# Optimization experiments

Measured on AMD Instinct MI355X. Metric: run time of the kernel, lower is better.

The kernel has to match this reference:

```python
import jax, jax.numpy as jnp
import numpy as np

BATCH, T, IN, OUT, N = 8, 2048, 512, 512, 512
DS = 1024  # temporal_downsampling


def setup_inputs() -> dict:
    key = jax.random.key(0)
    ks = jax.random.split(key, 8)
    x = jax.random.normal(ks[0], (BATCH, T, IN), dtype=jnp.float32)
    # LRU ring initialization of eigenvalues lambda = exp(-exp(nu_log) + i*exp(theta_log))
    r_min, r_max = 0.4, 0.99
    u1 = jax.random.uniform(ks[1], (N,), dtype=jnp.float32)
    u2 = jax.random.uniform(ks[2], (N,), dtype=jnp.float32)
    nu_log = jnp.log(-0.5 * jnp.log(u1 * (r_max**2 - r_min**2) + r_min**2))
    theta_log = jnp.log(u2 * (2.0 * np.pi) + 1e-6)
    lam_abs = jnp.exp(-jnp.exp(nu_log))
    gamma_log = jnp.log(jnp.sqrt(1.0 - lam_abs**2))  # input normalization
    B_re = jax.random.normal(ks[3], (N, IN), dtype=jnp.float32) / np.sqrt(2 * IN)
    B_im = jax.random.normal(ks[4], (N, IN), dtype=jnp.float32) / np.sqrt(2 * IN)
    C_re = jax.random.normal(ks[5], (OUT, N), dtype=jnp.float32) / np.sqrt(N)
    C_im = jax.random.normal(ks[6], (OUT, N), dtype=jnp.float32) / np.sqrt(N)
    D = jax.random.normal(ks[7], (OUT, IN), dtype=jnp.float32) / np.sqrt(IN)
    return {"x": x, "nu_log": nu_log, "theta_log": theta_log, "gamma_log": gamma_log,
            "B_re": B_re, "B_im": B_im, "C_re": C_re, "C_im": C_im, "D": D}


def reference(x, nu_log, theta_log, gamma_log, B_re, B_im, C_re, C_im, D):
    # diagonal complex recurrence: h_t = lam * h_{t-1} + gamma * B x_t
    lam = jnp.exp(-jnp.exp(nu_log) + 1j * jnp.exp(theta_log))  # [N] complex64
    gamma = jnp.exp(gamma_log)  # [N]
    # input projection (real GEMMs), then scale: Bu [b, t, n] complex
    Bu = (jnp.einsum('bti,ni->btn', x, B_re)
          + 1j * jnp.einsum('bti,ni->btn', x, B_im)) * gamma
    a = jnp.broadcast_to(lam, Bu.shape)

    def combine(e1, e2):
        a1, b1 = e1
        a2, b2 = e2
        return a1 * a2, a2 * b1 + b2

    _, h = jax.lax.associative_scan(combine, (a, Bu), axis=1)  # h: [b, t, n]
    # y_t = Re(C h_t) + D x_t
    y = (jnp.einsum('btn,on->bto', h.real, C_re)
         - jnp.einsum('btn,on->bto', h.imag, C_im)
         + jnp.einsum('bti,oi->bto', x, D))
    # causal temporal downsampling: keep last DS steps
    return y[:, -DS:]
```

## Files before the change

kernel.cpp:

```cpp
#include <hip/hip_runtime.h>
#include <hip/hip_bf16.h>

typedef __attribute__((ext_vector_type(8))) short bf16x8;
typedef __attribute__((ext_vector_type(16))) float f32x16;

static __device__ __forceinline__ short f2bf(float f) {
    __hip_bfloat16 h = __float2bfloat16(f);
    return *reinterpret_cast<short*>(&h);
}
static __device__ __forceinline__ float bflo(unsigned v) {
    unsigned u = v << 16;
    return *reinterpret_cast<float*>(&u);
}
static __device__ __forceinline__ float bfhi(unsigned v) {
    unsigned u = v & 0xffff0000u;
    return *reinterpret_cast<float*>(&u);
}
static __device__ __forceinline__ unsigned pack2bf(float lo, float hi) {
    return (unsigned)(unsigned short)f2bf(lo) | ((unsigned)(unsigned short)f2bf(hi) << 16);
}

static __device__ __forceinline__ void gload16(const void* g, void* l) {
    __builtin_amdgcn_global_load_lds(
        (const __attribute__((address_space(1))) void*)g,
        (__attribute__((address_space(3))) void*)l, 16, 0, 0);
}

#define BATCH 8
#define TSEQ  2048
#define DS    1024
#define NIN   512
#define NOUT  512
#define NSTATE 512
#define WARM  768
#define TW    (TSEQ - WARM)
#define M1 (BATCH * TW)
#define N1 (2 * NSTATE)
#define K1 NIN
#define M2 (BATCH * DS)
#define N2 NOUT
#define KH 1024
#define K2 (3 * NSTATE)

#define PREP_A 512
#define PREP_B (N1 * K1)
#define PREP_C (N2 * K2)
#define PREP_D (M1 * K1 / 4)
#define PREP_TOT (PREP_A + PREP_B + PREP_C + PREP_D)
__global__ void k_prep(const float* __restrict__ nu_log,
                       const float* __restrict__ theta_log,
                       const float* __restrict__ gamma_log,
                       const float* __restrict__ B_re,
                       const float* __restrict__ B_im,
                       const float* __restrict__ C_re,
                       const float* __restrict__ C_im,
                       const float* __restrict__ D,
                       const float* __restrict__ x,
                       float* __restrict__ consts,
                       short* __restrict__ Bcat,
                       short* __restrict__ Wcat,
                       short* __restrict__ xb) {
    int idx = blockIdx.x * 256 + threadIdx.x;
    if (idx >= PREP_A + PREP_B + PREP_C) {
        int e  = (idx - PREP_A - PREP_B - PREP_C) * 4;
        int m  = e >> 9;
        int i  = e & 511;
        int b  = m / TW;
        int tt = m - b * TW;
        const float4 v = *reinterpret_cast<const float4*>(
            &x[((size_t)(b * TSEQ + WARM + tt) << 9) + i]);
        union { short s[4]; uint2 u; } pk;
        pk.s[0] = f2bf(v.x); pk.s[1] = f2bf(v.y);
        pk.s[2] = f2bf(v.z); pk.s[3] = f2bf(v.w);
        *reinterpret_cast<uint2*>(&xb[e]) = pk.u;
    } else if (idx < PREP_A) {
        int n = idx;
        float mag = expf(-expf(nu_log[n]));
        float th  = expf(theta_log[n]);
        float lre = mag * cosf(th);
        float lim = mag * sinf(th);
        consts[n]          = lre;
        consts[NSTATE + n] = lim;
        float pr = lre, pi = lim;
#pragma unroll
        for (int s = 0; s < 5; ++s) {
            float nr = pr * pr - pi * pi;
            float ni = 2.0f * pr * pi;
            pr = nr; pi = ni;
        }
        consts[2 * NSTATE + n] = pr;
        consts[3 * NSTATE + n] = pi;
    } else if (idx < PREP_A + PREP_B) {
        int e  = idx - PREP_A;
        int nn = e >> 9;
        int i  = e & 511;
        int n  = nn >> 1;
        float g = expf(gamma_log[n]);
        float v = ((nn & 1) ? B_im[n * NIN + i] : B_re[n * NIN + i]) * g;
        Bcat[e] = f2bf(v);
    } else {
        int e = idx - PREP_A - PREP_B;
        int o = e / K2;
        int k = e - o * K2;
        float v;
        if (k < 2 * NSTATE) {
            int n = k >> 1;
            v = (k & 1) ? -C_im[o * NSTATE + n] : C_re[o * NSTATE + n];
        } else {
            v = D[o * NIN + (k - 2 * NSTATE)];
        }
        Wcat[e] = f2bf(v);
    }
}

template <int TBM, int TBN, typename OutT, bool MIXED>
__global__ __launch_bounds__(256)
void gemm_bt(const short* __restrict__ A, const short* __restrict__ B,
             const short* __restrict__ A2, OutT* __restrict__ C,
             int M, int N, int K, int strideA) {
    constexpr int MI = TBM / 64;
    constexpr int NJ = TBN / 64;
    constexpr int PA = TBM / 32;
    constexpr int PB = TBN / 32;
    __shared__ short As[TBM][64];
    __shared__ short Bs[TBN][64];
    const int tid  = threadIdx.x;
    const int bm   = blockIdx.y * TBM;
    const int bn   = blockIdx.x * TBN;
    const int wave = tid >> 6;
    const int lane = tid & 63;
    const int wr   = (wave >> 1) * (TBM / 2);
    const int wc   = (wave & 1) * (TBN / 2);
    const int rr   = lane & 31;
    const int kh   = (lane >> 5) * 8;
    const int rsw  = (rr & 7) << 3;

    const int srow = tid >> 3;
    const int scol = (((tid & 7) ^ (srow & 7)) << 3);
    const int r0   = bm + srow;
    const short* ga0 = A + (size_t)r0 * strideA + scol;
    const short* gb0 = B + (size_t)(bn + srow) * K + scol;
    const short* ga2 = nullptr;
    if constexpr (MIXED)
        ga2 = A2 + ((size_t)((r0 >> 10) * TW + (TW - DS) + (r0 & 1023))) * NSTATE + scol;
    short* la0 = &As[0][0] + wave * 512;
    short* lb0 = &Bs[0][0] + wave * 512;

    f32x16 acc[MI][NJ] = {};

    for (int k0 = 0; k0 < K; k0 += 64) {
        if constexpr (MIXED) {
            if (k0 >= KH) {
#pragma unroll
                for (int p = 0; p < PA; ++p)
                    gload16(ga2 + (size_t)p * 32 * NSTATE + (k0 - KH), la0 + p * 2048);
            } else {
#pragma unroll
                for (int p = 0; p < PA; ++p)
                    gload16(ga0 + (size_t)p * 32 * strideA + k0, la0 + p * 2048);
            }
        } else {
#pragma unroll
            for (int p = 0; p < PA; ++p)
                gload16(ga0 + (size_t)p * 32 * strideA + k0, la0 + p * 2048);
        }
#pragma unroll
        for (int p = 0; p < PB; ++p)
            gload16(gb0 + (size_t)p * 32 * K + k0, lb0 + p * 2048);
        __syncthreads();
#pragma unroll
        for (int kk = 0; kk < 64; kk += 16) {
            bf16x8 a[MI], b[NJ];
#pragma unroll
            for (int i = 0; i < MI; ++i)
                a[i] = *reinterpret_cast<const bf16x8*>(&As[wr + i * 32 + rr][(kk + kh) ^ rsw]);
#pragma unroll
            for (int j = 0; j < NJ; ++j)
                b[j] = *reinterpret_cast<const bf16x8*>(&Bs[wc + j * 32 + rr][(kk + kh) ^ rsw]);
#pragma unroll
            for (int i = 0; i < MI; ++i)
#pragma unroll
                for (int j = 0; j < NJ; ++j)
                    acc[i][j] = __builtin_amdgcn_mfma_f32_32x32x16_bf16(a[i], b[j], acc[i][j], 0, 0, 0);
        }
        __syncthreads();
    }

    const int rbase = (lane >> 5) * 4;
#pragma unroll
    for (int i = 0; i < MI; ++i)
#pragma unroll
        for (int j = 0; j < NJ; ++j)
#pragma unroll
            for (int r = 0; r < 16; ++r) {
                int row = bm + wr + i * 32 + (r & 3) + 8 * (r >> 2) + rbase;
                int col = bn + wc + j * 32 + rr;
                if constexpr (sizeof(OutT) == 2)
                    C[(size_t)row * N + col] = (OutT)f2bf(acc[i][j][r]);
                else
                    C[(size_t)row * N + col] = acc[i][j][r];
            }
}

#define NCH (TW / 32)
#define WCH ((TW - DS) / 32)
__global__ __launch_bounds__(NCH * 8)
void scan_kernel(const unsigned* __restrict__ Bu,
                 const float* __restrict__ consts,
                 short* __restrict__ Hcat) {
    __shared__ float S_re[NCH][16], S_im[NCH][16];
    __shared__ float I_re[NCH][16], I_im[NCH][16];
    const int tid = threadIdx.x;
    const int jj  = tid & 7;
    const int c   = tid >> 3;
    const int b   = blockIdx.x >> 5;
    const int g   = blockIdx.x & 31;
    const int n0  = g * 16 + jj * 2;

    const float lre0 = consts[n0],                lim0 = consts[NSTATE + n0];
    const float lre1 = consts[n0 + 1],            lim1 = consts[NSTATE + n0 + 1];
    const float pre0 = consts[2 * NSTATE + n0],   pim0 = consts[3 * NSTATE + n0];
    const float pre1 = consts[2 * NSTATE + n0+1], pim1 = consts[3 * NSTATE + n0+1];

    const unsigned* base = Bu + ((size_t)(b * TW + c * 32)) * NSTATE + n0;

    float s0r = 0.f, s0i = 0.f, s1r = 0.f, s1i = 0.f;
#pragma unroll 4
    for (int t = 0; t < 32; ++t) {
        uint2 v = *reinterpret_cast<const uint2*>(&base[(size_t)t * NSTATE]);
        float t0r = lre0 * s0r - lim0 * s0i + bflo(v.x);
        float t0i = lre0 * s0i + lim0 * s0r + bfhi(v.x);
        s0r = t0r; s0i = t0i;
        float t1r = lre1 * s1r - lim1 * s1i + bflo(v.y);
        float t1i = lre1 * s1i + lim1 * s1r + bfhi(v.y);
        s1r = t1r; s1i = t1i;
    }
    S_re[c][jj * 2]     = s0r;  S_im[c][jj * 2]     = s0i;
    S_re[c][jj * 2 + 1] = s1r;  S_im[c][jj * 2 + 1] = s1i;
    __syncthreads();

    if (c == 0) {
        float c0r = 0.f, c0i = 0.f, c1r = 0.f, c1i = 0.f;
#pragma unroll
        for (int cc = 0; cc < NCH; ++cc) {
            I_re[cc][jj * 2]     = c0r;  I_im[cc][jj * 2]     = c0i;
            I_re[cc][jj * 2 + 1] = c1r;  I_im[cc][jj * 2 + 1] = c1i;
            float t0r = pre0 * c0r - pim0 * c0i + S_re[cc][jj * 2];
            float t0i = pre0 * c0i + pim0 * c0r + S_im[cc][jj * 2];
            c0r = t0r; c0i = t0i;
            float t1r = pre1 * c1r - pim1 * c1i + S_re[cc][jj * 2 + 1];
            float t1i = pre1 * c1i + pim1 * c1r + S_im[cc][jj * 2 + 1];
            c1r = t1r; c1i = t1i;
        }
    }
    __syncthreads();

    if (c >= WCH) {
        float h0r = I_re[c][jj * 2],     h0i = I_im[c][jj * 2];
        float h1r = I_re[c][jj * 2 + 1], h1i = I_im[c][jj * 2 + 1];
        short* outbase = Hcat + (size_t)(b * DS + (c - WCH) * 32) * KH;
#pragma unroll 4
        for (int t = 0; t < 32; ++t) {
            uint2 v = *reinterpret_cast<const uint2*>(&base[(size_t)t * NSTATE]);
            float t0r = lre0 * h0r - lim0 * h0i + bflo(v.x);
            float t0i = lre0 * h0i + lim0 * h0r + bfhi(v.x);
            h0r = t0r; h0i = t0i;
            float t1r = lre1 * h1r - lim1 * h1i + bflo(v.y);
            float t1i = lre1 * h1i + lim1 * h1r + bfhi(v.y);
            h1r = t1r; h1i = t1i;
            uint2 w;
            w.x = pack2bf(h0r, h0i);
            w.y = pack2bf(h1r, h1i);
            *reinterpret_cast<uint2*>(&outbase[(size_t)t * KH + 2 * n0]) = w;
        }
    }
}

extern "C" void kernel_launch(void* const* d_in, const int* in_sizes, int n_in,
                              void* d_out, int out_size, void* d_ws, size_t ws_size,
                              hipStream_t stream) {
    const float* x         = (const float*)d_in[0];
    const float* nu_log    = (const float*)d_in[1];
    const float* theta_log = (const float*)d_in[2];
    const float* gamma_log = (const float*)d_in[3];
    const float* B_re      = (const float*)d_in[4];
    const float* B_im      = (const float*)d_in[5];
    const float* C_re      = (const float*)d_in[6];
    const float* C_im      = (const float*)d_in[7];
    const float* D         = (const float*)d_in[8];

    char* ws = (char*)d_ws;
    float* consts = (float*)ws;
    short* Bcat   = (short*)(ws + 8192);
    short* Wcat   = (short*)(ws + 1056768);
    short* xb     = (short*)(ws + 2629632);
    short* Hcat   = (short*)(ws + 13115392);
    short* Bu     = (short*)(ws + 29892608);
    float* y      = (float*)d_out;

    hipLaunchKernelGGL(k_prep, dim3(PREP_TOT / 256), dim3(256), 0, stream,
                       nu_log, theta_log, gamma_log, B_re, B_im, C_re, C_im, D, x,
                       consts, Bcat, Wcat, xb);

    hipLaunchKernelGGL((gemm_bt<128, 128, short, false>), dim3(N1 / 128, M1 / 128), dim3(256), 0, stream,
                       xb, Bcat, nullptr, Bu, M1, N1, K1, K1);

    hipLaunchKernelGGL(scan_kernel, dim3(256), dim3(NCH * 8), 0, stream,
                       (const unsigned*)Bu, consts, Hcat);

    hipLaunchKernelGGL((gemm_bt<64, 128, float, true>), dim3(N2 / 128, M2 / 64), dim3(256), 0, stream,
                       Hcat, Wcat, xb, y, M2, N2, K2, KH);
}
```

Before: 75.87 us.

## Fuse prep, GEMMs and scan into one cooperative persistent kernel

Replaces the four kernel launches with a single cooperative kernel of 512 blocks that runs the prep, input GEMM, chunked scan and output GEMM as phases separated by grid-wide syncs. The aim is to remove launch gaps and tail effects between stages. The scan chunk length also changes from 32 to 40 (32 chunks over the 1280-step window), and lambda^40 is built as lambda^32 times lambda^8. Risks are grid-sync overhead, the 128x128 GEMM phase no longer mapping one tile per block (640 tiles on 512 blocks), and the scan phase using only half the grid.

```diff
diff --git a/kernel.cpp b/kernel.cpp
--- a/kernel.cpp
+++ b/kernel.cpp
@@ -1,5 +1,8 @@
 #include <hip/hip_runtime.h>
 #include <hip/hip_bf16.h>
+#include <hip/hip_cooperative_groups.h>
+
+namespace cg = cooperative_groups;
 
 typedef __attribute__((ext_vector_type(8))) short bf16x8;
 typedef __attribute__((ext_vector_type(16))) float f32x16;
@@ -19,7 +22,6 @@
 static __device__ __forceinline__ unsigned pack2bf(float lo, float hi) {
     return (unsigned)(unsigned short)f2bf(lo) | ((unsigned)(unsigned short)f2bf(hi) << 16);
 }
-
 static __device__ __forceinline__ void gload16(const void* g, void* l) {
     __builtin_amdgcn_global_load_lds(
         (const __attribute__((address_space(1))) void*)g,
@@ -42,91 +44,30 @@
 #define KH 1024
 #define K2 (3 * NSTATE)
 
+#define GRID  512
+#define CHUNK 40
+#define NCH   32
+#define OUTSKIP (TW - DS)
+
 #define PREP_A 512
 #define PREP_B (N1 * K1)
 #define PREP_C (N2 * K2)
 #define PREP_D (M1 * K1 / 4)
 #define PREP_TOT (PREP_A + PREP_B + PREP_C + PREP_D)
-__global__ void k_prep(const float* __restrict__ nu_log,
-                       const float* __restrict__ theta_log,
-                       const float* __restrict__ gamma_log,
-                       const float* __restrict__ B_re,
-                       const float* __restrict__ B_im,
-                       const float* __restrict__ C_re,
-                       const float* __restrict__ C_im,
-                       const float* __restrict__ D,
-                       const float* __restrict__ x,
-                       float* __restrict__ consts,
-                       short* __restrict__ Bcat,
-                       short* __restrict__ Wcat,
-                       short* __restrict__ xb) {
-    int idx = blockIdx.x * 256 + threadIdx.x;
-    if (idx >= PREP_A + PREP_B + PREP_C) {
-        int e  = (idx - PREP_A - PREP_B - PREP_C) * 4;
-        int m  = e >> 9;
-        int i  = e & 511;
-        int b  = m / TW;
-        int tt = m - b * TW;
-        const float4 v = *reinterpret_cast<const float4*>(
-            &x[((size_t)(b * TSEQ + WARM + tt) << 9) + i]);
-        union { short s[4]; uint2 u; } pk;
-        pk.s[0] = f2bf(v.x); pk.s[1] = f2bf(v.y);
-        pk.s[2] = f2bf(v.z); pk.s[3] = f2bf(v.w);
-        *reinterpret_cast<uint2*>(&xb[e]) = pk.u;
-    } else if (idx < PREP_A) {
-        int n = idx;
-        float mag = expf(-expf(nu_log[n]));
-        float th  = expf(theta_log[n]);
-        float lre = mag * cosf(th);
-        float lim = mag * sinf(th);
-        consts[n]          = lre;
-        consts[NSTATE + n] = lim;
-        float pr = lre, pi = lim;
-#pragma unroll
-        for (int s = 0; s < 5; ++s) {
-            float nr = pr * pr - pi * pi;
-            float ni = 2.0f * pr * pi;
-            pr = nr; pi = ni;
-        }
-        consts[2 * NSTATE + n] = pr;
-        consts[3 * NSTATE + n] = pi;
-    } else if (idx < PREP_A + PREP_B) {
-        int e  = idx - PREP_A;
-        int nn = e >> 9;
-        int i  = e & 511;
-        int n  = nn >> 1;
-        float g = expf(gamma_log[n]);
-        float v = ((nn & 1) ? B_im[n * NIN + i] : B_re[n * NIN + i]) * g;
-        Bcat[e] = f2bf(v);
-    } else {
-        int e = idx - PREP_A - PREP_B;
-        int o = e / K2;
-        int k = e - o * K2;
-        float v;
-        if (k < 2 * NSTATE) {
-            int n = k >> 1;
-            v = (k & 1) ? -C_im[o * NSTATE + n] : C_re[o * NSTATE + n];
-        } else {
-            v = D[o * NIN + (k - 2 * NSTATE)];
-        }
-        Wcat[e] = f2bf(v);
-    }
-}
 
 template <int TBM, int TBN, typename OutT, bool MIXED>
-__global__ __launch_bounds__(256)
-void gemm_bt(const short* __restrict__ A, const short* __restrict__ B,
-             const short* __restrict__ A2, OutT* __restrict__ C,
-             int M, int N, int K, int strideA) {
+static __device__ __forceinline__
+void gemm_tile(const short* __restrict__ A, const short* __restrict__ B,
+               const short* __restrict__ A2, OutT* __restrict__ C,
+               int N, int K, int strideA, int bx, int by, char* smem, int tid) {
     constexpr int MI = TBM / 64;
     constexpr int NJ = TBN / 64;
     constexpr int PA = TBM / 32;
     constexpr int PB = TBN / 32;
-    __shared__ short As[TBM][64];
-    __shared__ short Bs[TBN][64];
-    const int tid  = threadIdx.x;
-    const int bm   = blockIdx.y * TBM;
-    const int bn   = blockIdx.x * TBN;
+    short (*As)[64] = (short (*)[64])smem;
+    short (*Bs)[64] = (short (*)[64])(smem + TBM * 128);
+    const int bm   = by * TBM;
+    const int bn   = bx * TBN;
     const int wave = tid >> 6;
     const int lane = tid & 63;
     const int wr   = (wave >> 1) * (TBM / 2);
@@ -143,8 +84,8 @@
     const short* ga2 = nullptr;
     if constexpr (MIXED)
         ga2 = A2 + ((size_t)((r0 >> 10) * TW + (TW - DS) + (r0 & 1023))) * NSTATE + scol;
-    short* la0 = &As[0][0] + wave * 512;
-    short* lb0 = &Bs[0][0] + wave * 512;
+    short* la0 = (short*)smem + wave * 512;
+    short* lb0 = (short*)(smem + TBM * 128) + wave * 512;
 
     f32x16 acc[MI][NJ] = {};
 
@@ -202,78 +143,162 @@
             }
 }
 
-#define NCH (TW / 32)
-#define WCH ((TW - DS) / 32)
-__global__ __launch_bounds__(NCH * 8)
-void scan_kernel(const unsigned* __restrict__ Bu,
-                 const float* __restrict__ consts,
-                 short* __restrict__ Hcat) {
-    __shared__ float S_re[NCH][16], S_im[NCH][16];
-    __shared__ float I_re[NCH][16], I_im[NCH][16];
+__global__ __launch_bounds__(256, 2)
+void fused_lru(const float* __restrict__ nu_log, const float* __restrict__ theta_log,
+               const float* __restrict__ gamma_log,
+               const float* __restrict__ B_re, const float* __restrict__ B_im,
+               const float* __restrict__ C_re, const float* __restrict__ C_im,
+               const float* __restrict__ D, const float* __restrict__ x,
+               float* __restrict__ consts, short* __restrict__ Bcat,
+               short* __restrict__ Wcat, short* __restrict__ xb,
+               short* __restrict__ Hcat, short* __restrict__ Bu,
+               float* __restrict__ y) {
+    __shared__ char smem[32768];
     const int tid = threadIdx.x;
-    const int jj  = tid & 7;
-    const int c   = tid >> 3;
-    const int b   = blockIdx.x >> 5;
-    const int g   = blockIdx.x & 31;
-    const int n0  = g * 16 + jj * 2;
-
-    const float lre0 = consts[n0],                lim0 = consts[NSTATE + n0];
-    const float lre1 = consts[n0 + 1],            lim1 = consts[NSTATE + n0 + 1];
-    const float pre0 = consts[2 * NSTATE + n0],   pim0 = consts[3 * NSTATE + n0];
-    const float pre1 = consts[2 * NSTATE + n0+1], pim1 = consts[3 * NSTATE + n0+1];
-
-    const unsigned* base = Bu + ((size_t)(b * TW + c * 32)) * NSTATE + n0;
-
-    float s0r = 0.f, s0i = 0.f, s1r = 0.f, s1i = 0.f;
+    const int bid = blockIdx.x;
+
+    for (int idx = bid * 256 + tid; idx < PREP_TOT; idx += GRID * 256) {
+        if (idx >= PREP_A + PREP_B + PREP_C) {
+            int e  = (idx - PREP_A - PREP_B - PREP_C) * 4;
+            int m  = e >> 9;
+            int i  = e & 511;
+            int b  = m / TW;
+            int tt = m - b * TW;
+            const float4 v = *reinterpret_cast<const float4*>(
+                &x[((size_t)(b * TSEQ + WARM + tt) << 9) + i]);
+            union { short s[4]; uint2 u; } pk;
+            pk.s[0] = f2bf(v.x); pk.s[1] = f2bf(v.y);
+            pk.s[2] = f2bf(v.z); pk.s[3] = f2bf(v.w);
+            *reinterpret_cast<uint2*>(&xb[e]) = pk.u;
+        } else if (idx < PREP_A) {
+            int n = idx;
+            float mag = expf(-expf(nu_log[n]));
+            float th  = expf(theta_log[n]);
+            float lre = mag * cosf(th);
+            float lim = mag * sinf(th);
+            consts[n]          = lre;
+            consts[NSTATE + n] = lim;
+            float pr = lre, pi = lim;
+#pragma unroll
+            for (int s = 0; s < 3; ++s) {
+                float nr = pr * pr - pi * pi;
+                float ni = 2.0f * pr * pi;
+                pr = nr; pi = ni;
+            }
+            float l8r = pr, l8i = pi;
+#pragma unroll
+            for (int s = 0; s < 2; ++s) {
+                float nr = pr * pr - pi * pi;
+                float ni = 2.0f * pr * pi;
+                pr = nr; pi = ni;
+            }
+            consts[2 * NSTATE + n] = pr * l8r - pi * l8i;
+            consts[3 * NSTATE + n] = pr * l8i + pi * l8r;
+        } else if (idx < PREP_A + PREP_B) {
+            int e  = idx - PREP_A;
+            int nn = e >> 9;
+            int i  = e & 511;
+            int n  = nn >> 1;
+            float g = expf(gamma_log[n]);
+            float v = ((nn & 1) ? B_im[n * NIN + i] : B_re[n * NIN + i]) * g;
+            Bcat[e] = f2bf(v);
+        } else {
+            int e = idx - PREP_A - PREP_B;
+            int o = e / K2;
+            int k = e - o * K2;
+            float v;
+            if (k < 2 * NSTATE) {
+                int n = k >> 1;
+                v = (k & 1) ? -C_im[o * NSTATE + n] : C_re[o * NSTATE + n];
+            } else {
+                v = D[o * NIN + (k - 2 * NSTATE)];
+            }
+            Wcat[e] = f2bf(v);
+        }
+    }
+    cg::this_grid().sync();
+
+    for (int t = bid; t < (N1 / 128) * (M1 / 128); t += GRID)
+        gemm_tile<128, 128, short, false>(xb, Bcat, nullptr, Bu, N1, K1, K1,
+                                          t & 7, t >> 3, smem, tid);
+    cg::this_grid().sync();
+
+    if (bid < 256) {
+        float* S_re = (float*)smem;
+        float* S_im = S_re + NCH * 16;
+        float* I_re = S_im + NCH * 16;
+        float* I_im = I_re + NCH * 16;
+        const int jj = tid & 7;
+        const int c  = tid >> 3;
+        const int b  = bid >> 5;
+        const int g  = bid & 31;
+        const int n0 = g * 16 + jj * 2;
+
+        const float lre0 = consts[n0],                lim0 = consts[NSTATE + n0];
+        const float lre1 = consts[n0 + 1],            lim1 = consts[NSTATE + n0 + 1];
+        const float pre0 = consts[2 * NSTATE + n0],   pim0 = consts[3 * NSTATE + n0];
+        const float pre1 = consts[2 * NSTATE + n0+1], pim1 = consts[3 * NSTATE + n0+1];
+
+        const unsigned* base = (const unsigned*)Bu + ((size_t)(b * TW + c * CHUNK)) * NSTATE + n0;
+
+        float s0r = 0.f, s0i = 0.f, s1r = 0.f, s1i = 0.f;
 #pragma unroll 4
-    for (int t = 0; t < 32; ++t) {
-        uint2 v = *reinterpret_cast<const uint2*>(&base[(size_t)t * NSTATE]);
-        float t0r = lre0 * s0r - lim0 * s0i + bflo(v.x);
-        float t0i = lre0 * s0i + lim0 * s0r + bfhi(v.x);
-        s0r = t0r; s0i = t0i;
-        float t1r = lre1 * s1r - lim1 * s1i + bflo(v.y);
-        float t1i = lre1 * s1i + lim1 * s1r + bfhi(v.y);
-        s1r = t1r; s1i = t1i;
+        for (int t = 0; t < CHUNK; ++t) {
+            uint2 v = *reinterpret_cast<const uint2*>(&base[(size_t)t * NSTATE]);
+            float t0r = lre0 * s0r - lim0 * s0i + bflo(v.x);
+            float t0i = lre0 * s0i + lim0 * s0r + bfhi(v.x);
+            s0r = t0r; s0i = t0i;
+            float t1r = lre1 * s1r - lim1 * s1i + bflo(v.y);
+            float t1i = lre1 * s1i + lim1 * s1r + bfhi(v.y);
+            s1r = t1r; s1i = t1i;
+        }
+        S_re[c * 16 + jj * 2]     = s0r;  S_im[c * 16 + jj * 2]     = s0i;
+        S_re[c * 16 + jj * 2 + 1] = s1r;  S_im[c * 16 + jj * 2 + 1] = s1i;
+        __syncthreads();
+
+        if (c == 0) {
+            float c0r = 0.f, c0i = 0.f, c1r = 0.f, c1i = 0.f;
+#pragma unroll
+            for (int cc = 0; cc < NCH; ++cc) {
+                I_re[cc * 16 + jj * 2]     = c0r;  I_im[cc * 16 + jj * 2]     = c0i;
+                I_re[cc * 16 + jj * 2 + 1] = c1r;  I_im[cc * 16 + jj * 2 + 1] = c1i;
+                float t0r = pre0 * c0r - pim0 * c0i + S_re[cc * 16 + jj * 2];
+                float t0i = pre0 * c0i + pim0 * c0r + S_im[cc * 16 + jj * 2];
+                c0r = t0r; c0i = t0i;
+                float t1r = pre1 * c1r - pim1 * c1i + S_re[cc * 16 + jj * 2 + 1];
+                float t1i = pre1 * c1i + pim1 * c1r + S_im[cc * 16 + jj * 2 + 1];
+                c1r = t1r; c1i = t1i;
+            }
+        }
+        __syncthreads();
+
+        if (c >= OUTSKIP / CHUNK) {
+            float h0r = I_re[c * 16 + jj * 2],     h0i = I_im[c * 16 + jj * 2];
+            float h1r = I_re[c * 16 + jj * 2 + 1], h1i = I_im[c * 16 + jj * 2 + 1];
+            const int sbase = c * CHUNK - OUTSKIP;
+#pragma unroll 4
+            for (int t = 0; t < CHUNK; ++t) {
+                uint2 v = *reinterpret_cast<const uint2*>(&base[(size_t)t * NSTATE]);
+                float t0r = lre0 * h0r - lim0 * h0i + bflo(v.x);
+                float t0i = lre0 * h0i + lim0 * h0r + bfhi(v.x);
+                h0r = t0r; h0i = t0i;
+                float t1r = lre1 * h1r - lim1 * h1i + bflo(v.y);
+                float t1i = lre1 * h1i + lim1 * h1r + bfhi(v.y);
+                h1r = t1r; h1i = t1i;
+                int srow = sbase + t;
+                if (srow >= 0) {
+                    uint2 w;
+                    w.x = pack2bf(h0r, h0i);
+                    w.y = pack2bf(h1r, h1i);
+                    *reinterpret_cast<uint2*>(&Hcat[(size_t)(b * DS + srow) * KH + 2 * n0]) = w;
+                }
+            }
+        }
     }
-    S_re[c][jj * 2]     = s0r;  S_im[c][jj * 2]     = s0i;
-    S_re[c][jj * 2 + 1] = s1r;  S_im[c][jj * 2 + 1] = s1i;
-    __syncthreads();
-
-    if (c == 0) {
-        float c0r = 0.f, c0i = 0.f, c1r = 0.f, c1i = 0.f;
-#pragma unroll
-        for (int cc = 0; cc < NCH; ++cc) {
-            I_re[cc][jj * 2]     = c0r;  I_im[cc][jj * 2]     = c0i;
-            I_re[cc][jj * 2 + 1] = c1r;  I_im[cc][jj * 2 + 1] = c1i;
-            float t0r = pre0 * c0r - pim0 * c0i + S_re[cc][jj * 2];
-            float t0i = pre0 * c0i + pim0 * c0r + S_im[cc][jj * 2];
-            c0r = t0r; c0i = t0i;
-            float t1r = pre1 * c1r - pim1 * c1i + S_re[cc][jj * 2 + 1];
-            float t1i = pre1 * c1i + pim1 * c1r + S_im[cc][jj * 2 + 1];
-            c1r = t1r; c1i = t1i;
-        }
-    }
-    __syncthreads();
-
-    if (c >= WCH) {
-        float h0r = I_re[c][jj * 2],     h0i = I_im[c][jj * 2];
-        float h1r = I_re[c][jj * 2 + 1], h1i = I_im[c][jj * 2 + 1];
-        short* outbase = Hcat + (size_t)(b * DS + (c - WCH) * 32) * KH;
-#pragma unroll 4
-        for (int t = 0; t < 32; ++t) {
-            uint2 v = *reinterpret_cast<const uint2*>(&base[(size_t)t * NSTATE]);
-            float t0r = lre0 * h0r - lim0 * h0i + bflo(v.x);
-            float t0i = lre0 * h0i + lim0 * h0r + bfhi(v.x);
-            h0r = t0r; h0i = t0i;
-            float t1r = lre1 * h1r - lim1 * h1i + bflo(v.y);
-            float t1i = lre1 * h1i + lim1 * h1r + bfhi(v.y);
-            h1r = t1r; h1i = t1i;
-            uint2 w;
-            w.x = pack2bf(h0r, h0i);
-            w.y = pack2bf(h1r, h1i);
-            *reinterpret_cast<uint2*>(&outbase[(size_t)t * KH + 2 * n0]) = w;
-        }
-    }
+    cg::this_grid().sync();
+
+    gemm_tile<64, 128, float, true>(Hcat, Wcat, xb, y, N2, K2, KH,
+                                    bid & 3, bid >> 2, smem, tid);
 }
 
 extern "C" void kernel_launch(void* const* d_in, const int* in_sizes, int n_in,
@@ -298,16 +323,13 @@
     short* Bu     = (short*)(ws + 29892608);
     float* y      = (float*)d_out;
 
-    hipLaunchKernelGGL(k_prep, dim3(PREP_TOT / 256), dim3(256), 0, stream,
-                       nu_log, theta_log, gamma_log, B_re, B_im, C_re, C_im, D, x,
-                       consts, Bcat, Wcat, xb);
-
-    hipLaunchKernelGGL((gemm_bt<128, 128, short, false>), dim3(N1 / 128, M1 / 128), dim3(256), 0, stream,
-                       xb, Bcat, nullptr, Bu, M1, N1, K1, K1);
-
-    hipLaunchKernelGGL(scan_kernel, dim3(256), dim3(NCH * 8), 0, stream,
-                       (const unsigned*)Bu, consts, Hcat);
-
-    hipLaunchKernelGGL((gemm_bt<64, 128, float, true>), dim3(N2 / 128, M2 / 64), dim3(256), 0, stream,
-                       Hcat, Wcat, xb, y, M2, N2, K2, KH);
-}
+    void* args[] = {
+        (void*)&nu_log, (void*)&theta_log, (void*)&gamma_log,
+        (void*)&B_re, (void*)&B_im, (void*)&C_re, (void*)&C_im,
+        (void*)&D, (void*)&x,
+        (void*)&consts, (void*)&Bcat, (void*)&Wcat, (void*)&xb,
+        (void*)&Hcat, (void*)&Bu, (void*)&y
+    };
+    hipLaunchCooperativeKernel((const void*)fused_lru, dim3(GRID), dim3(256),
+                               args, 0, stream);
+}
```

Measured after the change: 269.9 us. +255.8%, slower.
